# Performance work log

Hardware: AMD Instinct MI355X
Metric: run time of the kernel (lower is better)

## Reference

```python
import jax, jax.numpy as jnp
import numpy as np
from jax import lax

PAIRS = ((0, 1), (1, 2), (2, 3), (3, 0))


def _apply_1q(state, U, w):
    # state: (N,2,2,2,2); wire w lives at axis w+1
    state = jnp.moveaxis(state, w + 1, -1)
    if U.ndim == 2:  # shared gate across batch
        state = jnp.einsum('ij,...j->...i', U, state)
    else:            # per-batch gate (encoder), U: (N,2,2)
        state = jnp.einsum('nij,n...j->n...i', U, state)
    return jnp.moveaxis(state, -1, w + 1)


def _ry_mat(theta):
    # torchquantum RY: [[cos(t/2), -sin(t/2)], [sin(t/2), cos(t/2)]]
    h = theta * 0.5
    c, s = jnp.cos(h), jnp.sin(h)
    return jnp.stack([jnp.stack([c, -s], -1), jnp.stack([s, c], -1)], -2).astype(jnp.complex64)


def _rz_mat(theta):
    # torchquantum RZ: diag(e^{-i t/2}, e^{+i t/2})
    h = (theta * 0.5).astype(jnp.complex64)
    e0, e1 = jnp.exp(-1j * h), jnp.exp(1j * h)
    z = jnp.zeros_like(e0)
    return jnp.stack([jnp.stack([e0, z], -1), jnp.stack([z, e1], -1)], -2)


def _cnot(state, c, t):
    st = jnp.moveaxis(state, (c + 1, t + 1), (-2, -1))
    st = jnp.stack([st[..., 0, :], st[..., 1, ::-1]], axis=-2)
    return jnp.moveaxis(st, (-2, -1), (c + 1, t + 1))


def _ansatz(state, p, a, b):
    state = _apply_1q(state, _ry_mat(p[0]), a)
    state = _apply_1q(state, _rz_mat(p[1]), a)
    state = _apply_1q(state, _ry_mat(p[2]), b)
    state = _apply_1q(state, _rz_mat(p[3]), b)
    state = _cnot(state, a, b)
    state = _apply_1q(state, _ry_mat(p[4]), a)
    state = _apply_1q(state, _rz_mat(p[5]), a)
    state = _apply_1q(state, _ry_mat(p[6]), b)
    return state


def _circuit(angles, qp):
    # angles: (N,4) in [0,pi]; qp: (2,7). Returns <Z_w> per wire: (N,4)
    N = angles.shape[0]
    state = jnp.zeros((N, 2, 2, 2, 2), jnp.complex64).at[:, 0, 0, 0, 0].set(1.0)
    for w in range(4):  # GeneralEncoder: RY(x_w) on wire w
        state = _apply_1q(state, _ry_mat(angles[:, w]), w)
    for layer in range(2):
        for (a, b) in PAIRS:
            state = _ansatz(state, qp[layer], a, b)
    probs = state.real ** 2 + state.imag ** 2
    exps = []
    for w in range(4):
        axes = tuple(ax for ax in range(1, 5) if ax != w + 1)
        m = probs.sum(axis=axes)  # (N,2)
        exps.append(m[:, 0] - m[:, 1])
    return jnp.stack(exps, axis=-1)


def _conv(x, w, b):
    y = lax.conv_general_dilated(x, w, (1, 1), 'SAME',
                                 dimension_numbers=('NCHW', 'OIHW', 'NCHW'))
    return y + b[None, :, None, None]


def _pool(x):
    return lax.reduce_window(x, -jnp.inf, lax.max, (1, 1, 2, 2), (1, 1, 2, 2), 'VALID')


def setup_inputs() -> dict:
    key = jax.random.key(0)
    ks = jax.random.split(key, 16)
    r = lambda k, sh, sc=0.1: (jax.random.normal(k, sh, dtype=jnp.float32) * sc)
    return {
        'x': jax.random.normal(ks[0], (2048, 1, 28, 28), dtype=jnp.float32),
        'conv1_w': r(ks[1], (64, 1, 3, 3)), 'conv1_b': r(ks[2], (64,)),
        'conv2_w': r(ks[3], (16, 64, 3, 3)), 'conv2_b': r(ks[4], (16,)),
        'conv3_w': r(ks[5], (4, 16, 3, 3)), 'conv3_b': r(ks[6], (4,)),
        'q_params': jax.random.uniform(ks[7], (2, 7), dtype=jnp.float32),
        'fc1_w': r(ks[8], (64, 196)), 'fc1_b': r(ks[9], (64,)),
        'fc2_w': r(ks[10], (128, 64)), 'fc2_b': r(ks[11], (128,)),
        'fc3_w': r(ks[12], (64, 128)), 'fc3_b': r(ks[13], (64,)),
        'fc4_w': r(ks[14], (10, 64)), 'fc4_b': r(ks[15], (10,)),
    }


def reference(x, conv1_w, conv1_b, conv2_w, conv2_b, conv3_w, conv3_b,
              q_params, fc1_w, fc1_b, fc2_w, fc2_b, fc3_w, fc3_b, fc4_w, fc4_b):
    h = _pool(jax.nn.relu(_conv(x, conv1_w, conv1_b)))       # (B,64,14,14)
    h = _pool(jax.nn.relu(_conv(h, conv2_w, conv2_b)))       # (B,16,7,7)
    h = jax.nn.leaky_relu(_conv(h, conv3_w, conv3_b), 0.01)  # (B,4,7,7)
    B, C, H, W = h.shape
    # 1x1 patches: (B, H*W, C) -> flatten over patches
    patches = h.reshape(B, C, H * W).transpose(0, 2, 1).reshape(B * H * W, C)
    angles = jax.nn.sigmoid(patches) * np.float32(np.pi)
    q = _circuit(angles, q_params)            # (B*49, 4)
    q = q.reshape(B, H * W * C)               # (B, 196)
    h = jax.nn.relu(q @ fc1_w.T + fc1_b)
    h = h @ fc2_w.T + fc2_b
    h = jax.nn.relu(h @ fc3_w.T + fc3_b)
    return h @ fc4_w.T + fc4_b
```

## Files before the change

### kernel.cpp

```cpp
#include <hip/hip_runtime.h>
#include <hip/hip_bf16.h>
#include <math.h>

#define DEV __device__ __forceinline__

typedef __attribute__((ext_vector_type(4))) float f32x4;
typedef __attribute__((ext_vector_type(8))) short bf16x8;

DEV unsigned short f2bf(float v) {
    __hip_bfloat16 h = __float2bfloat16(v);
    return *reinterpret_cast<unsigned short*>(&h);
}
DEV unsigned pk2(float a, float b) {
    union { __hip_bfloat162 b2; unsigned u; } cv;
    cv.b2 = __float22bfloat162_rn(float2{a, b});
    return cv.u;
}

template<int B>
DEV void ry_b(float* sr, float* si, float c, float s) {
    #pragma unroll
    for (int i = 0; i < 16; ++i) if (!(i & B)) {
        int j = i | B;
        float r0 = sr[i], m0 = si[i], r1 = sr[j], m1 = si[j];
        sr[i] = c * r0 - s * r1;  si[i] = c * m0 - s * m1;
        sr[j] = s * r0 + c * r1;  si[j] = s * m0 + c * m1;
    }
}
template<int B>
DEV void rz_b(float* sr, float* si, float c, float s) {
    #pragma unroll
    for (int i = 0; i < 16; ++i) {
        float xr = sr[i], xi = si[i];
        if (!(i & B)) { sr[i] = c * xr + s * xi;  si[i] = c * xi - s * xr; }
        else          { sr[i] = c * xr - s * xi;  si[i] = c * xi + s * xr; }
    }
}
template<int BC, int BT>
DEV void cnot_b(float* sr, float* si) {
    #pragma unroll
    for (int i = 0; i < 16; ++i) if ((i & BC) && !(i & BT)) {
        int j = i | BT;
        float tr = sr[i]; sr[i] = sr[j]; sr[j] = tr;
        float ti = si[i]; si[i] = si[j]; si[j] = ti;
    }
}
template<int A, int Bw>
DEV void ansatz(float* sr, float* si, const float* cc, const float* ss) {
    constexpr int BA = 8 >> A, BB = 8 >> Bw;
    ry_b<BA>(sr, si, cc[0], ss[0]);
    rz_b<BA>(sr, si, cc[1], ss[1]);
    ry_b<BB>(sr, si, cc[2], ss[2]);
    rz_b<BB>(sr, si, cc[3], ss[3]);
    cnot_b<BA, BB>(sr, si);
    ry_b<BA>(sr, si, cc[4], ss[4]);
    rz_b<BA>(sr, si, cc[5], ss[5]);
    ry_b<BB>(sr, si, cc[6], ss[6]);
}

__global__ void prep_kernel(const float* __restrict__ w1,
                            const float* __restrict__ w2,
                            const float* __restrict__ w3,
                            const float* __restrict__ qp,
                            const float* __restrict__ fc1w,
                            const float* __restrict__ fc2w,
                            const float* __restrict__ fc3w,
                            const float* __restrict__ fc4w,
                            unsigned short* __restrict__ w1b,
                            unsigned short* __restrict__ w2b,
                            float* __restrict__ w3t,
                            float* __restrict__ ab,
                            float* __restrict__ fc1t,
                            float* __restrict__ fc2t,
                            float* __restrict__ fc3t,
                            float* __restrict__ fc4t)
{
    int t = blockIdx.x * blockDim.x + threadIdx.x;
    int NT = gridDim.x * blockDim.x;
    for (int i = t; i < 2048; i += NT) {
        int j = i & 7, oc = (i >> 3) & 63, fqq = i >> 9;
        int tap = fqq * 8 + j;
        w1b[i] = tap < 9 ? f2bf(w1[oc * 9 + tap]) : (unsigned short)0;
    }
    for (int i = t; i < 9216; i += NT) {
        int j = i & 7, oc = (i >> 3) & 15, fq = (i >> 7) & 3, f = i >> 9;
        int tap = f >> 1, kk = f & 1;
        int s = kk * 32 + fq * 8 + j;
        int ic = (s & 3) * 16 + (s >> 2);
        w2b[i] = f2bf(w2[(oc * 64 + ic) * 9 + tap]);
    }
    for (int i = t; i < 576; i += NT) {
        int c = i & 3, ch = (i >> 2) & 15, tap = i >> 6;
        w3t[i] = w3[(c * 16 + ch) * 9 + tap];
    }
    for (int i = t; i < 12544; i += NT) { int j = i / 196, k = i % 196; fc1t[k * 64 + j] = fc1w[i]; }
    for (int i = t; i < 8192;  i += NT) { int j = i / 64,  k = i % 64;  fc2t[k * 128 + j] = fc2w[i]; }
    for (int i = t; i < 8192;  i += NT) { int j = i / 128, k = i % 128; fc3t[k * 64 + j] = fc3w[i]; }
    for (int i = t; i < 640;   i += NT) { int j = i / 64,  k = i % 64;  fc4t[k * 10 + j] = fc4w[i]; }

    if (blockIdx.x == 0 && threadIdx.x < 16) {
        int b = threadIdx.x;
        float cs0[7], sn0[7], cs1[7], sn1[7];
        #pragma unroll
        for (int k = 0; k < 7; ++k) {
            __sincosf(qp[k] * 0.5f, &sn0[k], &cs0[k]);
            __sincosf(qp[7 + k] * 0.5f, &sn1[k], &cs1[k]);
        }
        float sr[16], si[16];
        #pragma unroll
        for (int i = 0; i < 16; ++i) { sr[i] = (i == b) ? 1.f : 0.f; si[i] = 0.f; }
        ansatz<0, 1>(sr, si, cs0, sn0);
        ansatz<1, 2>(sr, si, cs0, sn0);
        ansatz<2, 3>(sr, si, cs0, sn0);
        ansatz<3, 0>(sr, si, cs0, sn0);
        ansatz<0, 1>(sr, si, cs1, sn1);
        ansatz<1, 2>(sr, si, cs1, sn1);
        ansatz<2, 3>(sr, si, cs1, sn1);
        ansatz<3, 0>(sr, si, cs1, sn1);
        #pragma unroll
        for (int i = 0; i < 16; ++i) {
            ab[(i * 16 + b) * 2]     = sr[i];
            ab[(i * 16 + b) * 2 + 1] = si[i];
        }
    }
}

__global__ __launch_bounds__(256, 4) void conv12_kernel(
    const float* __restrict__ x,
    const float* __restrict__ b1, const unsigned short* __restrict__ w1b,
    const unsigned short* __restrict__ w2b,
    const float* __restrict__ b2, float* __restrict__ out2)
{
    __shared__ __align__(128) char lds_all[36864];
    float* pin = (float*)lds_all;
    char* in_b = lds_all + 4096;
    int t = threadIdx.x, lane = t & 63, wv = t >> 6;
    int fq = lane >> 4, fr = lane & 15;
    int n = blockIdx.x;

    bf16x8 bfrag[18];
    const bf16x8* wb = (const bf16x8*)w2b;
    #pragma unroll
    for (int f = 0; f < 18; ++f) bfrag[f] = wb[(f * 4 + fq) * 16 + fr];
    bf16x8 w1f[4];
    const bf16x8* wb1 = (const bf16x8*)w1b;
    float b1v[4];
    #pragma unroll
    for (int nt = 0; nt < 4; ++nt) {
        w1f[nt] = wb1[fq * 64 + nt * 16 + fr];
        b1v[nt] = b1[nt * 16 + fr];
    }
    float b2v = b2[fr];

    for (int i = t; i < 480; i += 256) {
        int ci = i >> 3, sub = i & 7;
        int g;
        if (ci < 16)      g = ci;
        else if (ci < 32) g = 240 + (ci - 16);
        else if (ci < 46) g = (ci - 31) * 16;
        else              g = (ci - 45) * 16 + 15;
        *(f32x4*)(in_b + g * 128 + sub * 16) = f32x4{0.f, 0.f, 0.f, 0.f};
    }
    for (int i = t; i < 1020; i += 256) pin[i] = 0.f;
    if (t < 128) {
        int cell = t >> 2, comp = t & 3;
        int pos;
        if (cell < 9)       pos = cell;
        else if (cell < 18) pos = 72 + (cell - 9);
        else if (cell < 25) pos = (cell - 17) * 9;
        else                pos = (cell - 24) * 9 + 8;
        *reinterpret_cast<float4*>(out2 + (size_t)n * 1296 + pos * 16 + comp * 4)
            = float4{0.f, 0.f, 0.f, 0.f};
    }
    __syncthreads();
    for (int i = t; i < 784; i += 256) pin[(i / 28 + 1) * 34 + (i % 28) + 1] = x[n * 784 + i];
    __syncthreads();

    for (int tile = wv; tile < 49; tile += 4) {
        int pooledA = tile * 4 + (fr >> 2);
        int pyA = pooledA / 14, pxA = pooledA - pyA * 14;
        int Y = 2 * pyA + ((fr >> 1) & 1), X = 2 * pxA + (fr & 1);
        const float* ap = pin + Y * 34 + X + (fq == 1 ? 70 : 0);
        float q0 = ap[0],  q1 = ap[1],  q2 = ap[2];
        float q3 = ap[34], q4 = ap[35], q5 = ap[36];
        float q6 = ap[68], q7 = ap[69];
        union { uint4 u; bf16x8 v; } A;
        A.u.x = pk2(q0, q1); A.u.y = pk2(q2, q3);
        A.u.z = pk2(q4, q5); A.u.w = pk2(q6, q7);

        f32x4 a0 = {0.f,0.f,0.f,0.f}, a1 = {0.f,0.f,0.f,0.f},
              a2 = {0.f,0.f,0.f,0.f}, a3 = {0.f,0.f,0.f,0.f};
        a0 = __builtin_amdgcn_mfma_f32_16x16x32_bf16(A.v, w1f[0], a0, 0, 0, 0);
        a1 = __builtin_amdgcn_mfma_f32_16x16x32_bf16(A.v, w1f[1], a1, 0, 0, 0);
        a2 = __builtin_amdgcn_mfma_f32_16x16x32_bf16(A.v, w1f[2], a2, 0, 0, 0);
        a3 = __builtin_amdgcn_mfma_f32_16x16x32_bf16(A.v, w1f[3], a3, 0, 0, 0);

        int pooled = tile * 4 + fq;
        int py = pooled / 14, px = pooled - py * 14;
        int grid = (py + 1) * 16 + (px + 1);
        unsigned swz = (unsigned)(grid & 7) << 4;
        float v0 = fmaxf(fmaxf(fmaxf(a0[0], a0[1]), fmaxf(a0[2], a0[3])) + b1v[0], 0.f);
        float v1 = fmaxf(fmaxf(fmaxf(a1[0], a1[1]), fmaxf(a1[2], a1[3])) + b1v[1], 0.f);
        float v2 = fmaxf(fmaxf(fmaxf(a2[0], a2[1]), fmaxf(a2[2], a2[3])) + b1v[2], 0.f);
        float v3 = fmaxf(fmaxf(fmaxf(a3[0], a3[1]), fmaxf(a3[2], a3[3])) + b1v[3], 0.f);
        uint2 w; w.x = pk2(v0, v1); w.y = pk2(v2, v3);
        *reinterpret_cast<uint2*>(in_b + (((unsigned)grid * 128 + (unsigned)fr * 8) ^ swz)) = w;
    }
    __syncthreads();

    for (int tile = wv; tile < 13; tile += 4) {
        f32x4 acc = {0.f, 0.f, 0.f, 0.f};
        int pv = tile * 4 + (fr >> 2); pv = pv > 48 ? 48 : pv;
        int sub = fr & 3;
        int y7 = pv / 7, x7 = pv - y7 * 7;
        int y = 2 * y7 + (sub >> 1), xx = 2 * x7 + (sub & 1);
        int g0 = y * 16 + xx;
        int vb = g0 * 128 + fq * 16;
        #pragma unroll
        for (int ky = 0; ky < 3; ++ky)
            #pragma unroll
            for (int kx = 0; kx < 3; ++kx) {
                int dg = ky * 16 + kx;
                int msk = ((g0 + dg) & 7) << 4;
                int lin = vb + dg * 128;
                bf16x8 a0 = *(const bf16x8*)(in_b + (lin ^ msk));
                acc = __builtin_amdgcn_mfma_f32_16x16x32_bf16(a0, bfrag[(ky * 3 + kx) * 2], acc, 0, 0, 0);
                bf16x8 a1 = *(const bf16x8*)(in_b + ((lin | 64) ^ msk));
                acc = __builtin_amdgcn_mfma_f32_16x16x32_bf16(a1, bfrag[(ky * 3 + kx) * 2 + 1], acc, 0, 0, 0);
            }
        int pooled2 = tile * 4 + fq;
        if (pooled2 < 49) {
            float m = fmaxf(fmaxf(acc[0], acc[1]), fmaxf(acc[2], acc[3]));
            int y9 = pooled2 / 7, x9 = pooled2 - y9 * 7;
            out2[(size_t)n * 1296 + ((y9 + 1) * 9 + (x9 + 1)) * 16 + fr] =
                fmaxf(m + b2v, 0.f);
        }
    }
}

__global__ __launch_bounds__(512) void qfc_kernel(
    const float* __restrict__ out2, const float* __restrict__ w3t,
    const float* __restrict__ b3, const float* __restrict__ ab,
    const float* __restrict__ fc1t, const float* __restrict__ fb1,
    const float* __restrict__ fc2t, const float* __restrict__ fb2,
    const float* __restrict__ fc3t, const float* __restrict__ fb3,
    const float* __restrict__ fc4t, const float* __restrict__ fb4,
    float* __restrict__ out)
{
    __shared__ float qr[8][196];
    __shared__ float h1[8][64], h2[8][128], h3[8][64];
    int t = threadIdx.x;
    int nb = blockIdx.x * 8;

    if (t < 392) {
        int nl = t / 49, p = t - nl * 49;
        int n = nb + nl;
        int py = p / 7, px = p - py * 7;
        const float* in = out2 + (size_t)n * 1296;

        float acc0 = b3[0], acc1 = b3[1], acc2 = b3[2], acc3 = b3[3];
        #pragma unroll
        for (int ky = 0; ky < 3; ++ky)
            #pragma unroll
            for (int kx = 0; kx < 3; ++kx) {
                const float* cp = in + ((py + ky) * 9 + (px + kx)) * 16;
                const float* wt = w3t + (ky * 3 + kx) * 64;
                #pragma unroll
                for (int icq = 0; icq < 4; ++icq) {
                    float4 v4 = *reinterpret_cast<const float4*>(cp + icq * 4);
                    const float* wq = wt + icq * 16;
                    acc0 = fmaf(wq[0],  v4.x, acc0); acc1 = fmaf(wq[1],  v4.x, acc1);
                    acc2 = fmaf(wq[2],  v4.x, acc2); acc3 = fmaf(wq[3],  v4.x, acc3);
                    acc0 = fmaf(wq[4],  v4.y, acc0); acc1 = fmaf(wq[5],  v4.y, acc1);
                    acc2 = fmaf(wq[6],  v4.y, acc2); acc3 = fmaf(wq[7],  v4.y, acc3);
                    acc0 = fmaf(wq[8],  v4.z, acc0); acc1 = fmaf(wq[9],  v4.z, acc1);
                    acc2 = fmaf(wq[10], v4.z, acc2); acc3 = fmaf(wq[11], v4.z, acc3);
                    acc0 = fmaf(wq[12], v4.w, acc0); acc1 = fmaf(wq[13], v4.w, acc1);
                    acc2 = fmaf(wq[14], v4.w, acc2); acc3 = fmaf(wq[15], v4.w, acc3);
                }
            }

        float cw[4], sw[4];
        {
            float az[4] = {acc0, acc1, acc2, acc3};
            #pragma unroll
            for (int c = 0; c < 4; ++c) {
                float z = az[c];
                z = z > 0.f ? z : 0.01f * z;
                float sg = 1.f / (1.f + __expf(-z));
                __sincosf(1.5707963267948966f * sg, &sw[c], &cw[c]);
            }
        }
        float p01[4] = { cw[0]*cw[1], cw[0]*sw[1], sw[0]*cw[1], sw[0]*sw[1] };
        float p23[4] = { cw[2]*cw[3], cw[2]*sw[3], sw[2]*cw[3], sw[2]*sw[3] };
        float v[16];
        #pragma unroll
        for (int i = 0; i < 16; ++i) v[i] = p01[i >> 2] * p23[i & 3];

        float e0 = 0.f, e1 = 0.f, e2 = 0.f, e3 = 0.f;
        #pragma unroll
        for (int i = 0; i < 16; ++i) {
            const float* row = ab + i * 32;
            float re = 0.f, im = 0.f;
            #pragma unroll
            for (int k = 0; k < 16; ++k) {
                re = fmaf(row[k * 2],     v[k], re);
                im = fmaf(row[k * 2 + 1], v[k], im);
            }
            float p2 = re * re + im * im;
            e0 += (i & 8) ? -p2 : p2;
            e1 += (i & 4) ? -p2 : p2;
            e2 += (i & 2) ? -p2 : p2;
            e3 += (i & 1) ? -p2 : p2;
        }
        *reinterpret_cast<float4*>(&qr[nl][p * 4]) = float4{e0, e1, e2, e3};
    }
    __syncthreads();

    int wv = t >> 6, lane = t & 63;
    int n = nb + wv;
    float a = fb1[lane];
    for (int k = 0; k < 196; ++k) a = fmaf(fc1t[k * 64 + lane], qr[wv][k], a);
    h1[wv][lane] = fmaxf(a, 0.f);
    __syncthreads();
    float a0 = fb2[lane], a1 = fb2[lane + 64];
    for (int k = 0; k < 64; ++k) {
        float vv = h1[wv][k];
        a0 = fmaf(fc2t[k * 128 + lane], vv, a0);
        a1 = fmaf(fc2t[k * 128 + lane + 64], vv, a1);
    }
    h2[wv][lane] = a0; h2[wv][lane + 64] = a1;
    __syncthreads();
    a = fb3[lane];
    for (int k = 0; k < 128; ++k) a = fmaf(fc3t[k * 64 + lane], h2[wv][k], a);
    h3[wv][lane] = fmaxf(a, 0.f);
    __syncthreads();
    if (lane < 10) {
        a = fb4[lane];
        for (int k = 0; k < 64; ++k) a = fmaf(fc4t[k * 10 + lane], h3[wv][k], a);
        out[n * 10 + lane] = a;
    }
}

extern "C" void kernel_launch(void* const* d_in, const int* in_sizes, int n_in,
                              void* d_out, int out_size, void* d_ws, size_t ws_size,
                              hipStream_t stream) {
    const float* x      = (const float*)d_in[0];
    const float* c1w    = (const float*)d_in[1];
    const float* c1b    = (const float*)d_in[2];
    const float* c2w    = (const float*)d_in[3];
    const float* c2b    = (const float*)d_in[4];
    const float* c3w    = (const float*)d_in[5];
    const float* c3b    = (const float*)d_in[6];
    const float* qp     = (const float*)d_in[7];
    const float* fc1w   = (const float*)d_in[8];
    const float* fc1b   = (const float*)d_in[9];
    const float* fc2w   = (const float*)d_in[10];
    const float* fc2b   = (const float*)d_in[11];
    const float* fc3w   = (const float*)d_in[12];
    const float* fc3b   = (const float*)d_in[13];
    const float* fc4w   = (const float*)d_in[14];
    const float* fc4b   = (const float*)d_in[15];
    float* out = (float*)d_out;

    float* ws = (float*)d_ws;
    unsigned short* w2b = (unsigned short*)ws;
    unsigned short* w1b = (unsigned short*)(ws + 4608);
    float* w3t  = ws + 5632;
    float* abm  = ws + 6208;
    float* fc1t = ws + 6720;
    float* fc2t = fc1t + 12544;
    float* fc3t = fc2t + 8192;
    float* fc4t = fc3t + 8192;
    float* out2 = fc4t + 640;

    prep_kernel<<<40, 256, 0, stream>>>(c1w, c2w, c3w, qp, fc1w, fc2w, fc3w, fc4w,
                                        w1b, w2b, w3t, abm, fc1t, fc2t, fc3t, fc4t);
    conv12_kernel<<<2048, 256, 0, stream>>>(x, c1b, w1b, w2b, c2b, out2);
    qfc_kernel<<<256, 512, 0, stream>>>(out2, w3t, c3b, abm,
                                        fc1t, fc1b, fc2t, fc2b,
                                        fc3t, fc3b, fc4t, fc4b, out);
}
```

Measured before the change: 63.81 us.

## Fuse conv3 and quantum circuit into conv12 kernel, keep conv2 output in LDS

Conv2 results now stay in shared memory instead of being written to a global padded buffer. Conv3, the sigmoid/sincos encoding and the quantum expectation evaluation run in the same per-sample block, so only a 196-float vector per sample reaches global memory for a separate FC kernel. The quantum work is split four ways per patch with a reduction through LDS, which raises parallelism. The cost is more barriers and a longer per-block tail in the conv kernel, where many threads sit idle.

New measurement: 83.27 us. 1.31x slower.

```diff
diff --git a/kernel.cpp b/kernel.cpp
--- a/kernel.cpp
+++ b/kernel.cpp
@@ -68,7 +68,7 @@
                             const float* __restrict__ fc4w,
                             unsigned short* __restrict__ w1b,
                             unsigned short* __restrict__ w2b,
-                            float* __restrict__ w3t,
+                            float* __restrict__ w3c,
                             float* __restrict__ ab,
                             float* __restrict__ fc1t,
                             float* __restrict__ fc2t,
@@ -90,8 +90,8 @@
         w2b[i] = f2bf(w2[(oc * 64 + ic) * 9 + tap]);
     }
     for (int i = t; i < 576; i += NT) {
-        int c = i & 3, ch = (i >> 2) & 15, tap = i >> 6;
-        w3t[i] = w3[(c * 16 + ch) * 9 + tap];
+        int ic = i & 15, tap = (i >> 4) % 9, c = i / 144;
+        w3c[i] = w3[(c * 16 + ic) * 9 + tap];
     }
     for (int i = t; i < 12544; i += NT) { int j = i / 196, k = i % 196; fc1t[k * 64 + j] = fc1w[i]; }
     for (int i = t; i < 8192;  i += NT) { int j = i / 64,  k = i % 64;  fc2t[k * 128 + j] = fc2w[i]; }
@@ -125,15 +125,19 @@
     }
 }
 
-__global__ __launch_bounds__(256, 4) void conv12_kernel(
+__global__ __launch_bounds__(256, 4) void conv123q_kernel(
     const float* __restrict__ x,
     const float* __restrict__ b1, const unsigned short* __restrict__ w1b,
-    const unsigned short* __restrict__ w2b,
-    const float* __restrict__ b2, float* __restrict__ out2)
+    const unsigned short* __restrict__ w2b, const float* __restrict__ b2,
+    const float* __restrict__ w3c, const float* __restrict__ b3,
+    const float* __restrict__ ab, float* __restrict__ q)
 {
     __shared__ __align__(128) char lds_all[36864];
-    float* pin = (float*)lds_all;
-    char* in_b = lds_all + 4096;
+    float* pin  = (float*)lds_all;
+    char*  in_b = lds_all + 4096;
+    float* d2   = (float*)in_b;
+    float* part = (float*)(in_b + 8192);
+    float* cwsw = pin;
     int t = threadIdx.x, lane = t & 63, wv = t >> 6;
     int fq = lane >> 4, fr = lane & 15;
     int n = blockIdx.x;
@@ -162,16 +166,6 @@
         *(f32x4*)(in_b + g * 128 + sub * 16) = f32x4{0.f, 0.f, 0.f, 0.f};
     }
     for (int i = t; i < 1020; i += 256) pin[i] = 0.f;
-    if (t < 128) {
-        int cell = t >> 2, comp = t & 3;
-        int pos;
-        if (cell < 9)       pos = cell;
-        else if (cell < 18) pos = 72 + (cell - 9);
-        else if (cell < 25) pos = (cell - 17) * 9;
-        else                pos = (cell - 24) * 9 + 8;
-        *reinterpret_cast<float4*>(out2 + (size_t)n * 1296 + pos * 16 + comp * 4)
-            = float4{0.f, 0.f, 0.f, 0.f};
-    }
     __syncthreads();
     for (int i = t; i < 784; i += 256) pin[(i / 28 + 1) * 34 + (i % 28) + 1] = x[n * 784 + i];
     __syncthreads();
@@ -208,7 +202,11 @@
     }
     __syncthreads();
 
-    for (int tile = wv; tile < 13; tile += 4) {
+    float rr0 = 0.f, rr1 = 0.f, rr2 = 0.f, rr3 = 0.f;
+    #pragma unroll
+    for (int it = 0; it < 4; ++it) {
+        int tile = wv + it * 4;
+        if (tile >= 13) break;
         f32x4 acc = {0.f, 0.f, 0.f, 0.f};
         int pv = tile * 4 + (fr >> 2); pv = pv > 48 ? 48 : pv;
         int sub = fr & 3;
@@ -228,78 +226,77 @@
                 bf16x8 a1 = *(const bf16x8*)(in_b + ((lin | 64) ^ msk));
                 acc = __builtin_amdgcn_mfma_f32_16x16x32_bf16(a1, bfrag[(ky * 3 + kx) * 2 + 1], acc, 0, 0, 0);
             }
+        float m = fmaxf(fmaxf(fmaxf(acc[0], acc[1]), fmaxf(acc[2], acc[3])) + b2v, 0.f);
+        if (it == 0) rr0 = m; else if (it == 1) rr1 = m;
+        else if (it == 2) rr2 = m; else rr3 = m;
+    }
+    __syncthreads();
+
+    if (t < 128) {
+        int cell = t >> 2, comp = t & 3;
+        int pos;
+        if (cell < 9)       pos = cell;
+        else if (cell < 18) pos = 72 + (cell - 9);
+        else if (cell < 25) pos = (cell - 17) * 9;
+        else                pos = (cell - 24) * 9 + 8;
+        *(f32x4*)(d2 + pos * 16 + comp * 4) = f32x4{0.f, 0.f, 0.f, 0.f};
+    }
+    #pragma unroll
+    for (int it = 0; it < 4; ++it) {
+        int tile = wv + it * 4;
         int pooled2 = tile * 4 + fq;
-        if (pooled2 < 49) {
-            float m = fmaxf(fmaxf(acc[0], acc[1]), fmaxf(acc[2], acc[3]));
+        if (tile < 13 && pooled2 < 49) {
+            float m = (it == 0) ? rr0 : (it == 1) ? rr1 : (it == 2) ? rr2 : rr3;
             int y9 = pooled2 / 7, x9 = pooled2 - y9 * 7;
-            out2[(size_t)n * 1296 + ((y9 + 1) * 9 + (x9 + 1)) * 16 + fr] =
-                fmaxf(m + b2v, 0.f);
+            d2[((y9 + 1) * 9 + (x9 + 1)) * 16 + fr] = m;
         }
     }
-}
-
-__global__ __launch_bounds__(512) void qfc_kernel(
-    const float* __restrict__ out2, const float* __restrict__ w3t,
-    const float* __restrict__ b3, const float* __restrict__ ab,
-    const float* __restrict__ fc1t, const float* __restrict__ fb1,
-    const float* __restrict__ fc2t, const float* __restrict__ fb2,
-    const float* __restrict__ fc3t, const float* __restrict__ fb3,
-    const float* __restrict__ fc4t, const float* __restrict__ fb4,
-    float* __restrict__ out)
-{
-    __shared__ float qr[8][196];
-    __shared__ float h1[8][64], h2[8][128], h3[8][64];
-    int t = threadIdx.x;
-    int nb = blockIdx.x * 8;
-
-    if (t < 392) {
-        int nl = t / 49, p = t - nl * 49;
-        int n = nb + nl;
+    __syncthreads();
+
+    if (t < 196) {
+        int p = t >> 2, c = t & 3;
         int py = p / 7, px = p - py * 7;
-        const float* in = out2 + (size_t)n * 1296;
-
-        float acc0 = b3[0], acc1 = b3[1], acc2 = b3[2], acc3 = b3[3];
+        float acc = b3[c];
         #pragma unroll
         for (int ky = 0; ky < 3; ++ky)
             #pragma unroll
             for (int kx = 0; kx < 3; ++kx) {
-                const float* cp = in + ((py + ky) * 9 + (px + kx)) * 16;
-                const float* wt = w3t + (ky * 3 + kx) * 64;
+                const float* dp = d2 + ((py + ky) * 9 + (px + kx)) * 16;
+                const float* wp = w3c + (c * 9 + ky * 3 + kx) * 16;
                 #pragma unroll
                 for (int icq = 0; icq < 4; ++icq) {
-                    float4 v4 = *reinterpret_cast<const float4*>(cp + icq * 4);
-                    const float* wq = wt + icq * 16;
-                    acc0 = fmaf(wq[0],  v4.x, acc0); acc1 = fmaf(wq[1],  v4.x, acc1);
-                    acc2 = fmaf(wq[2],  v4.x, acc2); acc3 = fmaf(wq[3],  v4.x, acc3);
-                    acc0 = fmaf(wq[4],  v4.y, acc0); acc1 = fmaf(wq[5],  v4.y, acc1);
-                    acc2 = fmaf(wq[6],  v4.y, acc2); acc3 = fmaf(wq[7],  v4.y, acc3);
-                    acc0 = fmaf(wq[8],  v4.z, acc0); acc1 = fmaf(wq[9],  v4.z, acc1);
-                    acc2 = fmaf(wq[10], v4.z, acc2); acc3 = fmaf(wq[11], v4.z, acc3);
-                    acc0 = fmaf(wq[12], v4.w, acc0); acc1 = fmaf(wq[13], v4.w, acc1);
-                    acc2 = fmaf(wq[14], v4.w, acc2); acc3 = fmaf(wq[15], v4.w, acc3);
+                    float4 dv = *reinterpret_cast<const float4*>(dp + icq * 4);
+                    float4 wv4 = *reinterpret_cast<const float4*>(wp + icq * 4);
+                    acc = fmaf(wv4.x, dv.x, acc);
+                    acc = fmaf(wv4.y, dv.y, acc);
+                    acc = fmaf(wv4.z, dv.z, acc);
+                    acc = fmaf(wv4.w, dv.w, acc);
                 }
             }
-
-        float cw[4], sw[4];
-        {
-            float az[4] = {acc0, acc1, acc2, acc3};
-            #pragma unroll
-            for (int c = 0; c < 4; ++c) {
-                float z = az[c];
-                z = z > 0.f ? z : 0.01f * z;
-                float sg = 1.f / (1.f + __expf(-z));
-                __sincosf(1.5707963267948966f * sg, &sw[c], &cw[c]);
-            }
-        }
-        float p01[4] = { cw[0]*cw[1], cw[0]*sw[1], sw[0]*cw[1], sw[0]*sw[1] };
-        float p23[4] = { cw[2]*cw[3], cw[2]*sw[3], sw[2]*cw[3], sw[2]*sw[3] };
+        float z = acc > 0.f ? acc : 0.01f * acc;
+        float sg = 1.f / (1.f + __expf(-z));
+        float sv, cv;
+        __sincosf(1.5707963267948966f * sg, &sv, &cv);
+        *reinterpret_cast<float2*>(&cwsw[t * 2]) = float2{cv, sv};
+    }
+    __syncthreads();
+
+    if (t < 196) {
+        int p = t >> 2, qd = t & 3;
+        float2 c0 = *reinterpret_cast<const float2*>(&cwsw[(p * 4 + 0) * 2]);
+        float2 c1 = *reinterpret_cast<const float2*>(&cwsw[(p * 4 + 1) * 2]);
+        float2 c2 = *reinterpret_cast<const float2*>(&cwsw[(p * 4 + 2) * 2]);
+        float2 c3 = *reinterpret_cast<const float2*>(&cwsw[(p * 4 + 3) * 2]);
+        float p01[4] = { c0.x*c1.x, c0.x*c1.y, c0.y*c1.x, c0.y*c1.y };
+        float p23[4] = { c2.x*c3.x, c2.x*c3.y, c2.y*c3.x, c2.y*c3.y };
         float v[16];
         #pragma unroll
         for (int i = 0; i < 16; ++i) v[i] = p01[i >> 2] * p23[i & 3];
 
         float e0 = 0.f, e1 = 0.f, e2 = 0.f, e3 = 0.f;
         #pragma unroll
-        for (int i = 0; i < 16; ++i) {
+        for (int ii = 0; ii < 4; ++ii) {
+            int i = qd * 4 + ii;
             const float* row = ab + i * 32;
             float re = 0.f, im = 0.f;
             #pragma unroll
@@ -313,21 +310,46 @@
             e2 += (i & 2) ? -p2 : p2;
             e3 += (i & 1) ? -p2 : p2;
         }
-        *reinterpret_cast<float4*>(&qr[nl][p * 4]) = float4{e0, e1, e2, e3};
-    }
-    __syncthreads();
-
-    int wv = t >> 6, lane = t & 63;
-    int n = nb + wv;
+        *reinterpret_cast<float4*>(&part[t * 4]) = float4{e0, e1, e2, e3};
+    }
+    __syncthreads();
+
+    if (t < 49) {
+        float4 s0 = *reinterpret_cast<const float4*>(&part[(t * 4 + 0) * 4]);
+        float4 s1 = *reinterpret_cast<const float4*>(&part[(t * 4 + 1) * 4]);
+        float4 s2 = *reinterpret_cast<const float4*>(&part[(t * 4 + 2) * 4]);
+        float4 s3 = *reinterpret_cast<const float4*>(&part[(t * 4 + 3) * 4]);
+        float4 r;
+        r.x = s0.x + s1.x + s2.x + s3.x;
+        r.y = s0.y + s1.y + s2.y + s3.y;
+        r.z = s0.z + s1.z + s2.z + s3.z;
+        r.w = s0.w + s1.w + s2.w + s3.w;
+        *reinterpret_cast<float4*>(q + (size_t)n * 196 + t * 4) = r;
+    }
+}
+
+__global__ __launch_bounds__(512) void fc_kernel(
+    const float* __restrict__ q,
+    const float* __restrict__ fc1t, const float* __restrict__ fb1,
+    const float* __restrict__ fc2t, const float* __restrict__ fb2,
+    const float* __restrict__ fc3t, const float* __restrict__ fb3,
+    const float* __restrict__ fc4t, const float* __restrict__ fb4,
+    float* __restrict__ out)
+{
+    __shared__ float qr[8][196], h1[8][64], h2[8][128], h3[8][64];
+    int t = threadIdx.x, wv = t >> 6, lane = t & 63;
+    int n = blockIdx.x * 8 + wv;
+    for (int i = lane; i < 196; i += 64) qr[wv][i] = q[n * 196 + i];
+    __syncthreads();
     float a = fb1[lane];
     for (int k = 0; k < 196; ++k) a = fmaf(fc1t[k * 64 + lane], qr[wv][k], a);
     h1[wv][lane] = fmaxf(a, 0.f);
     __syncthreads();
     float a0 = fb2[lane], a1 = fb2[lane + 64];
     for (int k = 0; k < 64; ++k) {
-        float vv = h1[wv][k];
-        a0 = fmaf(fc2t[k * 128 + lane], vv, a0);
-        a1 = fmaf(fc2t[k * 128 + lane + 64], vv, a1);
+        float v = h1[wv][k];
+        a0 = fmaf(fc2t[k * 128 + lane], v, a0);
+        a1 = fmaf(fc2t[k * 128 + lane + 64], v, a1);
     }
     h2[wv][lane] = a0; h2[wv][lane + 64] = a1;
     __syncthreads();
@@ -366,18 +388,18 @@
     float* ws = (float*)d_ws;
     unsigned short* w2b = (unsigned short*)ws;
     unsigned short* w1b = (unsigned short*)(ws + 4608);
-    float* w3t  = ws + 5632;
+    float* w3c  = ws + 5632;
     float* abm  = ws + 6208;
     float* fc1t = ws + 6720;
     float* fc2t = fc1t + 12544;
     float* fc3t = fc2t + 8192;
     float* fc4t = fc3t + 8192;
-    float* out2 = fc4t + 640;
+    float* qbuf = fc4t + 640;
 
     prep_kernel<<<40, 256, 0, stream>>>(c1w, c2w, c3w, qp, fc1w, fc2w, fc3w, fc4w,
-                                        w1b, w2b, w3t, abm, fc1t, fc2t, fc3t, fc4t);
-    conv12_kernel<<<2048, 256, 0, stream>>>(x, c1b, w1b, w2b, c2b, out2);
-    qfc_kernel<<<256, 512, 0, stream>>>(out2, w3t, c3b, abm,
-                                        fc1t, fc1b, fc2t, fc2b,
-                                        fc3t, fc3b, fc4t, fc4b, out);
-}
+                                        w1b, w2b, w3c, abm, fc1t, fc2t, fc3t, fc4t);
+    conv123q_kernel<<<2048, 256, 0, stream>>>(x, c1b, w1b, w2b, c2b,
+                                              w3c, c3b, abm, qbuf);
+    fc_kernel<<<256, 512, 0, stream>>>(qbuf, fc1t, fc1b, fc2t, fc2b,
+                                       fc3t, fc3b, fc4t, fc4b, out);
+}
```
